# Kernel optimization log

Measured on AMD Instinct MI355X. Metric: run time of the kernel, lower is better.

Reference implementation:

```python
import jax, jax.numpy as jnp
import numpy as np

H = 512  # hidden_state_size

def _lstm_step(x, state, W, b):
    # state = cat(h, c), gates computed from cat(x, h) with a single fused [n, 4H] matmul
    h, c = state[:, :H], state[:, H:]
    z = jnp.concatenate([x, h], axis=1) @ W + b
    i, f, o, g = jnp.split(z, 4, axis=1)
    c_new = jax.nn.sigmoid(f) * c + jax.nn.sigmoid(i) * jnp.tanh(g)
    h_new = jax.nn.sigmoid(o) * jnp.tanh(c_new)
    return jnp.concatenate([h_new, c_new], axis=1)

def setup_inputs() -> dict:
    key = jax.random.key(0)
    ks = jax.random.split(key, 8)
    B, T, R, D, E, V = 128, 25, 100, 512, 512, 10000
    n0 = E + D + H  # cell0: cat(embed, pooled_cnn, h)
    n1 = 2 * D + H  # cell1: cat(h1[:, :D], attention_context, h)
    rn = lambda k, s, sc: jax.random.normal(k, s, dtype=jnp.float32) * sc
    return {
        "tokens": jax.random.randint(ks[0], (B, T), 0, V),
        "processed_cnn_features": rn(ks[1], (B, R, D), 1.0),
        "initial_hidden_state": rn(ks[2], (2, B, 2 * H), 1.0),
        "emb": rn(ks[3], (V, E), 1.0),
        "W0": rn(ks[4], (n0, 4 * H), 1.0 / np.sqrt(n0)),
        "b0": jnp.zeros((4 * H,), jnp.float32),
        "W1": rn(ks[5], (n1, 4 * H), 1.0 / np.sqrt(n1)),
        "b1": jnp.zeros((4 * H,), jnp.float32),
        "attn_W": rn(ks[6], (2 * H, R), 1.0 / np.sqrt(2 * H)),
        "attn_b": jnp.zeros((R,), jnp.float32),
        "out_W": rn(ks[7], (D, V), 1.0 / np.sqrt(D)),
        "out_b": jnp.zeros((V,), jnp.float32),
    }

def reference(tokens, processed_cnn_features, initial_hidden_state, emb,
              W0, b0, W1, b1, attn_W, attn_b, out_W, out_b):
    D = processed_cnn_features.shape[2]
    embeddings = emb[tokens]  # [B, T, E]
    # MaxPool1d(10) over regions then take window 0 == max over first 10 regions (loop-invariant)
    cnn_pooled = processed_cnn_features[:, :10, :].max(axis=1)  # [B, D]

    def step(carry, x_t):
        s0, s1 = carry
        s0 = _lstm_step(jnp.concatenate([x_t, cnn_pooled], axis=1), s0, W0, b0)
        attn = jax.nn.softmax(s0 @ attn_W + attn_b, axis=1)            # [B, R]
        ctx = jnp.einsum('br,brd->bd', attn, processed_cnn_features)   # [B, D]
        s1 = _lstm_step(jnp.concatenate([s0[:, :D], ctx], axis=1), s1, W1, b1)
        logits = s1[:, :D] @ out_W + out_b                             # [B, V]
        return (s0, s1), logits

    (s0, s1), logits_t = jax.lax.scan(
        step, (initial_hidden_state[0], initial_hidden_state[1]),
        jnp.swapaxes(embeddings, 0, 1))
    logits = jnp.swapaxes(logits_t, 0, 1)  # [B, T, V]
    final_hidden = jnp.stack([s0, s1], axis=0)  # [2, B, 2H]
    return logits, final_hidden
```

## Files before the change

### kernel.cpp

```cpp
#include <hip/hip_runtime.h>
#include <math.h>

#define BB   128
#define TT   25
#define RR   100
#define DD   512
#define VV   10000
#define NG   2048
#define PAD  8

typedef short bf8   __attribute__((ext_vector_type(8)));
typedef float f32x4 __attribute__((ext_vector_type(4)));

__device__ __forceinline__ float sigm(float x) { return 1.f / (1.f + expf(-x)); }

__device__ __forceinline__ short f2bf(float f) {
  unsigned u = __float_as_uint(f);
  u += 0x7fffu + ((u >> 16) & 1u);
  return (short)(u >> 16);
}
__device__ __forceinline__ float bf2f(short h) {
  return __uint_as_float(((unsigned)(unsigned short)h) << 16);
}

__global__ __launch_bounds__(256) void k_init(const float* __restrict__ ihs,
                                              short* __restrict__ CCH0,
                                              short* __restrict__ CCH1,
                                              float* __restrict__ C0,
                                              float* __restrict__ C1,
                                              int* __restrict__ bar) {
  if (blockIdx.x == 0 && threadIdx.x == 0) { bar[0] = 0; bar[1] = 0; }
  int idx = blockIdx.x * 256 + threadIdx.x;
  int s = idx >> 17, r = idx & 131071, b = r >> 10, j = r & 1023;
  float v = ihs[idx];
  if (s == 0) {
    if (j < 512) CCH1[b * 1536 + j] = f2bf(v);
    else         C0[b * 512 + (j - 512)] = v;
  } else {
    if (j < 512) CCH0[b * 1536 + 1024 + j] = f2bf(v);
    else         C1[b * 512 + (j - 512)] = v;
  }
}

__global__ __launch_bounds__(256) void k_pool(const float* __restrict__ feat,
                                              float* __restrict__ pool) {
  int idx = blockIdx.x * 256 + threadIdx.x;
  int b = idx >> 9, d = idx & 511;
  float m = -3.4e38f;
  #pragma unroll
  for (int r = 0; r < 10; r++)
    m = fmaxf(m, feat[((size_t)b * RR + r) * 512 + d]);
  pool[idx] = m;
}

__global__ __launch_bounds__(256) void k_xin(const int* __restrict__ tok,
                                             const float* __restrict__ emb,
                                             const float* __restrict__ pool,
                                             short* __restrict__ xin) {
  int idx = blockIdx.x * 256 + threadIdx.x;
  int m = idx >> 10, k = idx & 1023;
  int t = m >> 7, b = m & 127;
  float v;
  if (k < 512) v = emb[(size_t)tok[b * TT + t] * 512 + k];
  else         v = pool[b * 512 + (k - 512)];
  xin[idx] = f2bf(v);
}

__global__ __launch_bounds__(256) void k_transpose(const float* __restrict__ in,
                                                   short* __restrict__ out,
                                                   int K, int N) {
  __shared__ float tile[32][33];
  int kt = blockIdx.y * 32, nt = blockIdx.x * 32;
  int tx = threadIdx.x & 31, ty = threadIdx.x >> 5;
  #pragma unroll
  for (int i = 0; i < 32; i += 8) {
    int k = kt + ty + i, n = nt + tx;
    tile[ty + i][tx] = (n < N) ? in[(size_t)k * N + n] : 0.f;
  }
  __syncthreads();
  #pragma unroll
  for (int i = 0; i < 32; i += 8) {
    int n = nt + ty + i, k = kt + tx;
    if (n < N) out[(size_t)n * K + k] = f2bf(tile[tx][ty + i]);
  }
}

__global__ __launch_bounds__(256) void k_transpose_f32(const float* __restrict__ in,
                                                       float* __restrict__ out,
                                                       int K, int N) {
  __shared__ float tile[32][33];
  int kt = blockIdx.y * 32, nt = blockIdx.x * 32;
  int tx = threadIdx.x & 31, ty = threadIdx.x >> 5;
  #pragma unroll
  for (int i = 0; i < 32; i += 8) {
    int k = kt + ty + i, n = nt + tx;
    tile[ty + i][tx] = (n < N) ? in[(size_t)k * N + n] : 0.f;
  }
  __syncthreads();
  #pragma unroll
  for (int i = 0; i < 32; i += 8) {
    int n = nt + ty + i, k = kt + tx;
    if (n < N) out[(size_t)n * K + k] = tile[tx][ty + i];
  }
}

__global__ __launch_bounds__(256) void gemm_mfma(
    const short* __restrict__ A, int lda,
    const short* __restrict__ BT, int ldb,
    const float* __restrict__ bias,
    float* __restrict__ C, int ldc,
    int N, int K, int mode) {
  __shared__ short As[128][64 + PAD];
  __shared__ short Bs[128][64 + PAD];
  const int tid = threadIdx.x;
  const int wv = tid >> 6, ln = tid & 63;
  const int m0 = blockIdx.y * 128, n0 = blockIdx.x * 128;
  const int mw = (wv & 1) * 64, nw = (wv >> 1) * 64;
  const int lrow = ln & 15, quad = ln >> 4, lk8 = quad * 8;

  f32x4 acc[4][4] = {};
  for (int k0 = 0; k0 < K; k0 += 64) {
    #pragma unroll
    for (int v = 0; v < 4; v++) {
      int f = v * 256 + tid, r = f >> 3, kk = (f & 7) * 8;
      *(uint4*)&As[r][kk] = *(const uint4*)&A[(size_t)(m0 + r) * lda + k0 + kk];
    }
    #pragma unroll
    for (int v = 0; v < 4; v++) {
      int f = v * 256 + tid, r = f >> 3, kk = (f & 7) * 8;
      int n = n0 + r;
      uint4 val{0, 0, 0, 0};
      if (n < N) val = *(const uint4*)&BT[(size_t)n * ldb + k0 + kk];
      *(uint4*)&Bs[r][kk] = val;
    }
    __syncthreads();
    #pragma unroll
    for (int ks = 0; ks < 64; ks += 32) {
      bf8 af[4], bf[4];
      #pragma unroll
      for (int i = 0; i < 4; i++)
        af[i] = *(const bf8*)&As[mw + i * 16 + lrow][ks + lk8];
      #pragma unroll
      for (int j = 0; j < 4; j++)
        bf[j] = *(const bf8*)&Bs[nw + j * 16 + lrow][ks + lk8];
      #pragma unroll
      for (int i = 0; i < 4; i++)
        #pragma unroll
        for (int j = 0; j < 4; j++)
          acc[i][j] = __builtin_amdgcn_mfma_f32_16x16x32_bf16(
              af[i], bf[j], acc[i][j], 0, 0, 0);
    }
    __syncthreads();
  }
  #pragma unroll
  for (int i = 0; i < 4; i++) {
    #pragma unroll
    for (int j = 0; j < 4; j++) {
      #pragma unroll
      for (int r = 0; r < 4; r++) {
        int m = m0 + mw + i * 16 + quad * 4 + r;
        int n = n0 + nw + j * 16 + lrow;
        if (n < N) {
          float v = acc[i][j][r] + (bias ? bias[n] : 0.f);
          if (mode == 0) C[(size_t)m * ldc + n] = v;
          else {
            int t = m >> 7, b = m & 127;
            C[(size_t)b * (TT * VV) + (size_t)t * VV + n] = v;
          }
        }
      }
    }
  }
}

#define LSTM_PHASE(APTR, BTPTR, KTOT, HAS_X, XROW, BIASP, CSTP, HDSTP,        \
                   H0FP, H1ATP)                                               \
  {                                                                           \
    f32x4 acc0 = {}, acc1 = {};                                               \
    for (int k0 = 0; k0 < (KTOT); k0 += 256) {                                \
      _Pragma("unroll")                                                       \
      for (int v = 0; v < 4; v++) {                          \
        int f = v * 256 + tid, r = f >> 5, c = (f & 31) * 8;                  \
        *(uint4*)&As[r][c] =                                                  \
            *(const uint4*)&(APTR)[(size_t)(m0 + r) * 1536 + k0 + c];         \
      }                                                                       \
      _Pragma("unroll")                                                       \
      for (int v = 0; v < 8; v++) {              \
        int f = v * 256 + tid, r = f >> 5, c = (f & 31) * 8;                  \
        int n = ((r >> 4) << 9) + j0 + (r & 15);                              \
        *(uint4*)&Bs[r][c] =                                                  \
            *(const uint4*)&(BTPTR)[(size_t)n * (KTOT) + k0 + c];             \
      }                                                                       \
      __syncthreads();                                                        \
      _Pragma("unroll")                                                       \
      for (int ks = 0; ks < 256; ks += 32) {        \
        bf8 a0 = *(const bf8*)&As[lrow][ks + lk8];                            \
        bf8 a1 = *(const bf8*)&As[16 + lrow][ks + lk8];                       \
        bf8 bb = *(const bf8*)&Bs[wv * 16 + lrow][ks + lk8];                  \
        acc0 = __builtin_amdgcn_mfma_f32_16x16x32_bf16(a0, bb, acc0, 0,0,0);  \
        acc1 = __builtin_amdgcn_mfma_f32_16x16x32_bf16(a1, bb, acc1, 0,0,0);  \
      }                                                                       \
      __syncthreads();                                                        \
    }                                                                         \
    _Pragma("unroll")                                                         \
    for (int r = 0; r < 4; r++) {                                             \
      zs[wv * 512 + (quad * 4 + r) * 16 + lrow] = acc0[r];                    \
      zs[wv * 512 + (16 + quad * 4 + r) * 16 + lrow] = acc1[r];               \
    }                                                                         \
    __syncthreads();                                                          \
    _Pragma("unroll")                                                         \
    for (int e = 0; e < 2; e++) {                  \
      int o = e * 256 + tid, mm = o >> 4, jj = o & 15;                        \
      int b = m0 + mm, j = j0 + jj;                                           \
      float zi = zs[mm * 16 + jj];                                            \
      float zf = zs[512 + mm * 16 + jj];                                      \
      float zo = zs[1024 + mm * 16 + jj];                                     \
      float zg = zs[1536 + mm * 16 + jj];                                     \
      if (HAS_X) {                                                            \
        const float* q = (XROW) + (size_t)b * NG + j;                         \
        zi += q[0]; zf += q[512]; zo += q[1024]; zg += q[1536];               \
      } else {                                                                \
        zi += (BIASP)[j];        zf += (BIASP)[512 + j];                      \
        zo += (BIASP)[1024 + j]; zg += (BIASP)[1536 + j];                     \
      }                                                                       \
      float c  = (CSTP)[b * 512 + j];                                         \
      float cn = sigm(zf) * c + sigm(zi) * tanhf(zg);                         \
      float hn = sigm(zo) * tanhf(cn);                                        \
      (CSTP)[b * 512 + j] = cn;                                               \
      short hb = f2bf(hn);                                                    \
      (HDSTP)[b * 1536 + j] = hb;                                             \
      if (H0FP)  ((float*)(H0FP))[b * 512 + j] = hn;                          \
      if (H1ATP) ((short*)(H1ATP))[(size_t)b * 512 + j] = hb;                 \
    }                                                                         \
    __syncthreads();                                                          \
  }

#define GSYNC()                                                               \
  {                                                                           \
    phase++;                                                                  \
    __syncthreads();                                                          \
    if (tid == 0) {                                                           \
      __threadfence();                                                        \
      atomicAdd(&bar[0], 1);                                                  \
      while (atomicAdd(&bar[0], 0) < phase * 128) {}                          \
      __threadfence();                                                        \
    }                                                                         \
    __syncthreads();                                                          \
  }

__global__ __launch_bounds__(256) void k_loop(
    const float* X0, const short* W0hT, const short* W1T, const float* b1,
    const float* aWT, const float* ab, const float* feat,
    short* CCH0, short* CCH1, float* C0, float* C1,
    float* H0F, short* H1A, int* bar) {
  __shared__ short As[32][264];
  __shared__ short Bs[64][264];
  __shared__ float zs[2048];
  const int tid = threadIdx.x, bid = blockIdx.x;
  const int m0 = (bid >> 5) * 32, j0 = (bid & 31) * 16;
  const int wv = tid >> 6, ln = tid & 63;
  const int lrow = ln & 15, quad = ln >> 4, lk8 = quad * 8;
  int phase = 0;

  LSTM_PHASE(CCH1, W0hT, 512, 1, X0, b1, C0, CCH0, H0F, (short*)0);
  GSYNC();

  #pragma unroll 1
  for (int t = 0; t < TT; t++) {
    short* CCHp = (t & 1) ? CCH1 : CCH0;
    short* CCHq = (t & 1) ? CCH0 : CCH1;

    {
      float* s0s = zs;
      float* sc  = zs + 1024;
      float* al  = zs + 1280;
      int b = bid;
      #pragma unroll
      for (int h = 0; h < 2; h++) {
        int j = h * 256 + tid;
        s0s[j]       = H0F[b * 512 + j];
        s0s[512 + j] = C0[b * 512 + j];
      }
      __syncthreads();
      if (tid < 200) {
        int r = tid >> 1, hf = tid & 1;
        const float4* wp = (const float4*)(aWT + (size_t)r * 1024 + hf * 512);
        const float4* sp = (const float4*)(s0s + hf * 512);
        float a2 = 0.f;
        #pragma unroll 8
        for (int k4 = 0; k4 < 128; k4++) {
          float4 wq = wp[k4], sq = sp[k4];
          a2 += wq.x * sq.x + wq.y * sq.y + wq.z * sq.z + wq.w * sq.w;
        }
        sc[tid] = a2;
      }
      __syncthreads();
      if (tid < 128) al[tid] = -3.4e38f;
      if (tid < 100) al[tid] = sc[2 * tid] + sc[2 * tid + 1] + ab[tid];
      __syncthreads();
      if (tid < 128) sc[tid] = al[tid];
      __syncthreads();
      for (int off = 64; off; off >>= 1) {
        if (tid < off) sc[tid] = fmaxf(sc[tid], sc[tid + off]);
        __syncthreads();
      }
      float mx = sc[0];
      __syncthreads();
      if (tid < 128) {
        float e = (tid < 100) ? expf(al[tid] - mx) : 0.f;
        al[tid] = e; sc[tid] = e;
      }
      __syncthreads();
      for (int off = 64; off; off >>= 1) {
        if (tid < off) sc[tid] += sc[tid + off];
        __syncthreads();
      }
      float inv = 1.f / sc[0];
      #pragma unroll
      for (int h = 0; h < 2; h++) {
        int d = h * 256 + tid;
        float a2 = 0.f;
        for (int r = 0; r < RR; r++)
          a2 += al[r] * feat[((size_t)b * RR + r) * 512 + d];
        CCHp[b * 1536 + 512 + d] = f2bf(a2 * inv);
      }
      __syncthreads();
    }
    GSYNC();

    LSTM_PHASE(CCHp, W1T, 1536, 0, X0, b1, C1, CCHq + 1024, (float*)0,
               H1A + (size_t)t * BB * DD);

    if (t + 1 < TT) {
      LSTM_PHASE(CCHp, W0hT, 512, 1, X0 + (size_t)(t + 1) * BB * NG, b1,
                 C0, CCHq, H0F, (short*)0);
    }
    GSYNC();
  }
}

__global__ __launch_bounds__(256) void k_final(
    const short* __restrict__ CCH0, const short* __restrict__ CCH1,
    const float* __restrict__ C0, const float* __restrict__ C1,
    float* __restrict__ out) {
  int idx = blockIdx.x * 256 + threadIdx.x;
  int s = idx >> 17, r = idx & 131071, b = r >> 10, j = r & 1023;
  float v;
  if (s == 0) v = (j < 512) ? bf2f(CCH0[b * 1536 + j])        : C0[b * 512 + j - 512];
  else        v = (j < 512) ? bf2f(CCH1[b * 1536 + 1024 + j]) : C1[b * 512 + j - 512];
  out[(size_t)BB * TT * VV + idx] = v;
}

extern "C" void kernel_launch(void* const* d_in, const int* in_sizes, int n_in,
                              void* d_out, int out_size, void* d_ws, size_t ws_size,
                              hipStream_t stream) {
  const int*   tok  = (const int*)  d_in[0];
  const float* feat = (const float*)d_in[1];
  const float* ihs  = (const float*)d_in[2];
  const float* emb  = (const float*)d_in[3];
  const float* W0   = (const float*)d_in[4];
  const float* b0   = (const float*)d_in[5];
  const float* W1   = (const float*)d_in[6];
  const float* b1   = (const float*)d_in[7];
  const float* aW   = (const float*)d_in[8];
  const float* ab   = (const float*)d_in[9];
  const float* oW   = (const float*)d_in[10];
  const float* ob   = (const float*)d_in[11];
  float* out = (float*)d_out;
  char*  w   = (char*)d_ws;

  short* XIN  = (short*)w;
  short* H1A  = (short*)w;
  float* X0   = (float*)(w + 6553600);
  float* POOL = (float*)(w + 32768000);
  short* CCH0 = (short*)(w + 33030144);
  short* CCH1 = (short*)(w + 33423360);
  float* C0   = (float*)(w + 33816576);
  float* C1   = (float*)(w + 34078720);
  float* H0F  = (float*)(w + 34340864);
  short* W0xT = (short*)(w + 34603008);
  short* W0hT = (short*)(w + 38797312);
  short* W1T  = (short*)(w + 40894464);
  short* oWT  = (short*)(w + 47185920);
  float* aWT  = (float*)(w + 57425920);
  int*   bar  = (int*)  (w + 57835520);

  k_init<<<1024, 256, 0, stream>>>(ihs, CCH0, CCH1, C0, C1, bar);
  k_pool<<<256, 256, 0, stream>>>(feat, POOL);
  k_xin<<<12800, 256, 0, stream>>>(tok, emb, POOL, XIN);

  k_transpose<<<dim3(64, 32), 256, 0, stream>>>(W0, W0xT, 1024, 2048);
  k_transpose<<<dim3(64, 16), 256, 0, stream>>>(W0 + 1024 * NG, W0hT, 512, 2048);
  k_transpose<<<dim3(64, 48), 256, 0, stream>>>(W1, W1T, 1536, 2048);
  k_transpose<<<dim3(313, 16), 256, 0, stream>>>(oW, oWT, 512, 10000);
  k_transpose_f32<<<dim3(4, 32), 256, 0, stream>>>(aW, aWT, 1024, 100);

  gemm_mfma<<<dim3(16, 25), 256, 0, stream>>>(
      XIN, 1024, W0xT, 1024, b0, X0, NG, NG, 1024, 0);

  k_loop<<<128, 256, 0, stream>>>(X0, W0hT, W1T, b1, aWT, ab, feat,
                                  CCH0, CCH1, C0, C1, H0F, H1A, bar);

  gemm_mfma<<<dim3(79, 25), 256, 0, stream>>>(
      H1A, 512, oWT, 512, ob, out, VV, VV, 512, 1);
  k_final<<<1024, 256, 0, stream>>>(CCH0, CCH1, C0, C1, out);
}
```

Baseline: 1.669 ms.

## Register-prefetch LSTM GEMM tiles, flag-based grid barrier, vectorized attention context

The LSTM gate GEMM now loads the next K-chunks of A and B into registers ahead of time (double-buffered), so global loads overlap with the MFMA work on the current chunk. The grid barrier drops the single contended atomic counter: each block writes its own padded flag with release semantics, and 128 threads poll all the flags with acquire loads. The attention-context reduction splits the regions across the four waves and uses float4 loads, then sums the partials through shared memory. Together these aim to cut global-load latency, barrier contention and uncoalesced access, at the cost of more registers, an extra shared buffer and a larger flag array.

```diff
diff --git a/kernel.cpp b/kernel.cpp
--- a/kernel.cpp
+++ b/kernel.cpp
@@ -29,8 +29,8 @@
                                               float* __restrict__ C0,
                                               float* __restrict__ C1,
                                               int* __restrict__ bar) {
-  if (blockIdx.x == 0 && threadIdx.x == 0) { bar[0] = 0; bar[1] = 0; }
   int idx = blockIdx.x * 256 + threadIdx.x;
+  if (idx < 2048) bar[idx] = 0;
   int s = idx >> 17, r = idx & 131071, b = r >> 10, j = r & 1023;
   float v = ihs[idx];
   if (s == 0) {
@@ -173,34 +173,67 @@
   }
 }
 
+#define LP_ISSUE(PA, PB, APTR, BTPTR, KTOT, KC)                               \
+    _Pragma("unroll")                                                         \
+    for (int v = 0; v < 4; v++) {                            \
+      int f = v * 256 + tid, r = f >> 5, cc = (f & 31) * 8;                   \
+      PA[v] = *(const uint4*)&(APTR)[(size_t)(m0 + r) * 1536 + (KC) + cc];    \
+    }                                                                         \
+    _Pragma("unroll")                                                         \
+    for (int v = 0; v < 8; v++) {                \
+      int f = v * 256 + tid, r = f >> 5, cc = (f & 31) * 8;                   \
+      int n = ((r >> 4) << 9) + j0 + (r & 15);                                \
+      PB[v] = *(const uint4*)&(BTPTR)[(size_t)n * (KTOT) + (KC) + cc];        \
+    }
+
+#define LP_STAGE(PA, PB)                                                      \
+    _Pragma("unroll")                                                         \
+    for (int v = 0; v < 4; v++) {                                             \
+      int f = v * 256 + tid, r = f >> 5, cc = (f & 31) * 8;                   \
+      *(uint4*)&As[r][cc] = PA[v];                                            \
+    }                                                                         \
+    _Pragma("unroll")                                                         \
+    for (int v = 0; v < 8; v++) {                                             \
+      int f = v * 256 + tid, r = f >> 5, cc = (f & 31) * 8;                   \
+      *(uint4*)&Bs[r][cc] = PB[v];                                            \
+    }                                                                         \
+    __syncthreads();
+
+#define LP_MFMA()                                                             \
+    _Pragma("unroll")                                                         \
+    for (int ks = 0; ks < 256; ks += 32) {          \
+      bf8 a0 = *(const bf8*)&As[lrow][ks + lk8];                              \
+      bf8 a1 = *(const bf8*)&As[16 + lrow][ks + lk8];                         \
+      bf8 bb = *(const bf8*)&Bs[wv * 16 + lrow][ks + lk8];                    \
+      acc0 = __builtin_amdgcn_mfma_f32_16x16x32_bf16(a0, bb, acc0, 0, 0, 0);  \
+      acc1 = __builtin_amdgcn_mfma_f32_16x16x32_bf16(a1, bb, acc1, 0, 0, 0);  \
+    }                                                                         \
+    __syncthreads();
+
 #define LSTM_PHASE(APTR, BTPTR, KTOT, HAS_X, XROW, BIASP, CSTP, HDSTP,        \
                    H0FP, H1ATP)                                               \
   {                                                                           \
     f32x4 acc0 = {}, acc1 = {};                                               \
-    for (int k0 = 0; k0 < (KTOT); k0 += 256) {                                \
-      _Pragma("unroll")                                                       \
-      for (int v = 0; v < 4; v++) {                          \
-        int f = v * 256 + tid, r = f >> 5, c = (f & 31) * 8;                  \
-        *(uint4*)&As[r][c] =                                                  \
-            *(const uint4*)&(APTR)[(size_t)(m0 + r) * 1536 + k0 + c];         \
-      }                                                                       \
-      _Pragma("unroll")                                                       \
-      for (int v = 0; v < 8; v++) {              \
-        int f = v * 256 + tid, r = f >> 5, c = (f & 31) * 8;                  \
-        int n = ((r >> 4) << 9) + j0 + (r & 15);                              \
-        *(uint4*)&Bs[r][c] =                                                  \
-            *(const uint4*)&(BTPTR)[(size_t)n * (KTOT) + k0 + c];             \
-      }                                                                       \
-      __syncthreads();                                                        \
-      _Pragma("unroll")                                                       \
-      for (int ks = 0; ks < 256; ks += 32) {        \
-        bf8 a0 = *(const bf8*)&As[lrow][ks + lk8];                            \
-        bf8 a1 = *(const bf8*)&As[16 + lrow][ks + lk8];                       \
-        bf8 bb = *(const bf8*)&Bs[wv * 16 + lrow][ks + lk8];                  \
-        acc0 = __builtin_amdgcn_mfma_f32_16x16x32_bf16(a0, bb, acc0, 0,0,0);  \
-        acc1 = __builtin_amdgcn_mfma_f32_16x16x32_bf16(a1, bb, acc1, 0,0,0);  \
-      }                                                                       \
-      __syncthreads();                                                        \
+    uint4 pa0[4], pb0[8], pa1[4], pb1[8];                                     \
+    LP_ISSUE(pa0, pb0, APTR, BTPTR, KTOT, 0)                                  \
+    LP_ISSUE(pa1, pb1, APTR, BTPTR, KTOT, 256)                                \
+    LP_STAGE(pa0, pb0)                                                        \
+    if ((KTOT) > 512) { LP_ISSUE(pa0, pb0, APTR, BTPTR, KTOT, 512) }          \
+    LP_MFMA()                                                                 \
+    LP_STAGE(pa1, pb1)                                                        \
+    if ((KTOT) > 512) { LP_ISSUE(pa1, pb1, APTR, BTPTR, KTOT, 768) }          \
+    LP_MFMA()                                                                 \
+    if ((KTOT) > 512) {                                                       \
+      LP_STAGE(pa0, pb0)                                                      \
+      LP_ISSUE(pa0, pb0, APTR, BTPTR, KTOT, 1024)                             \
+      LP_MFMA()                                                               \
+      LP_STAGE(pa1, pb1)                                                      \
+      LP_ISSUE(pa1, pb1, APTR, BTPTR, KTOT, 1280)                             \
+      LP_MFMA()                                                               \
+      LP_STAGE(pa0, pb0)                                                      \
+      LP_MFMA()                                                               \
+      LP_STAGE(pa1, pb1)                                                      \
+      LP_MFMA()                                                               \
     }                                                                         \
     _Pragma("unroll")                                                         \
     for (int r = 0; r < 4; r++) {                                             \
@@ -241,8 +274,12 @@
     __syncthreads();                                                          \
     if (tid == 0) {                                                           \
       __threadfence();                                                        \
-      atomicAdd(&bar[0], 1);                                                  \
-      while (atomicAdd(&bar[0], 0) < phase * 128) {}                          \
+      __hip_atomic_store(&bar[bid * 16], phase, __ATOMIC_RELEASE,             \
+                         __HIP_MEMORY_SCOPE_AGENT);                           \
+    }                                                                         \
+    if (tid < 128) {                                                          \
+      while (__hip_atomic_load(&bar[tid * 16], __ATOMIC_ACQUIRE,              \
+                               __HIP_MEMORY_SCOPE_AGENT) < phase) {}          \
       __threadfence();                                                        \
     }                                                                         \
     __syncthreads();                                                          \
@@ -256,6 +293,7 @@
   __shared__ short As[32][264];
   __shared__ short Bs[64][264];
   __shared__ float zs[2048];
+  __shared__ float attn_s[1408];
   const int tid = threadIdx.x, bid = blockIdx.x;
   const int m0 = (bid >> 5) * 32, j0 = (bid & 31) * 16;
   const int wv = tid >> 6, ln = tid & 63;
@@ -271,9 +309,9 @@
     short* CCHq = (t & 1) ? CCH0 : CCH1;
 
     {
-      float* s0s = zs;
-      float* sc  = zs + 1024;
-      float* al  = zs + 1280;
+      float* s0s = attn_s;
+      float* sc  = attn_s + 1024;
+      float* al  = attn_s + 1280;
       int b = bid;
       #pragma unroll
       for (int h = 0; h < 2; h++) {
@@ -316,13 +354,34 @@
         __syncthreads();
       }
       float inv = 1.f / sc[0];
-      #pragma unroll
-      for (int h = 0; h < 2; h++) {
-        int d = h * 256 + tid;
-        float a2 = 0.f;
-        for (int r = 0; r < RR; r++)
-          a2 += al[r] * feat[((size_t)b * RR + r) * 512 + d];
-        CCHp[b * 1536 + 512 + d] = f2bf(a2 * inv);
+      {
+        const float* fb = feat + (size_t)b * RR * 512;
+        f32x4 ac0 = {}, ac1 = {};
+        int rbase = wv * 25;
+        #pragma unroll 5
+        for (int ri = 0; ri < 25; ri++) {
+          int r = rbase + ri;
+          float a = al[r];
+          const float* row = fb + (size_t)r * 512;
+          float4 v0 = *(const float4*)&row[ln * 4];
+          float4 v1 = *(const float4*)&row[256 + ln * 4];
+          ac0[0] += a * v0.x; ac0[1] += a * v0.y;
+          ac0[2] += a * v0.z; ac0[3] += a * v0.w;
+          ac1[0] += a * v1.x; ac1[1] += a * v1.y;
+          ac1[2] += a * v1.z; ac1[3] += a * v1.w;
+        }
+        #pragma unroll
+        for (int k = 0; k < 4; k++) {
+          zs[wv * 512 + ln * 4 + k]       = ac0[k];
+          zs[wv * 512 + 256 + ln * 4 + k] = ac1[k];
+        }
+        __syncthreads();
+        #pragma unroll
+        for (int p = 0; p < 2; p++) {
+          int dd = p * 256 + tid;
+          float s = zs[dd] + zs[512 + dd] + zs[1024 + dd] + zs[1536 + dd];
+          CCHp[b * 1536 + 512 + dd] = f2bf(s * inv);
+        }
       }
       __syncthreads();
     }
```

After: 2.938 ms. +76.0%, slower.
